# Kernel optimization log

Measured on AMD Instinct MI355X. Metric: run time of the kernel, lower is better.

## Reference

```python
import jax, jax.numpy as jnp
import numpy as np

B, T, H = 64, 1024, 1024


def setup_inputs() -> dict:
    key = jax.random.key(0)
    ks = jax.random.split(key, 8)
    s = 1.0 / np.sqrt(H)
    return {
        "spatial_feats": jax.random.normal(ks[0], (B, T, H), dtype=jnp.float32),
        "hidden_state": jax.random.normal(ks[1], (B, H), dtype=jnp.float32),
        "W_enc": jax.random.uniform(ks[2], (H, H), jnp.float32, -s, s),
        "b_enc": jax.random.uniform(ks[3], (H,), jnp.float32, -s, s),
        "W_dec": jax.random.uniform(ks[4], (H, H), jnp.float32, -s, s),
        "b_dec": jax.random.uniform(ks[5], (H,), jnp.float32, -s, s),
        "w_score": jax.random.uniform(ks[6], (H,), jnp.float32, -s, s),
        "b_score": jax.random.uniform(ks[7], (), jnp.float32, -s, s),
    }


def reference(spatial_feats, hidden_state, W_enc, b_enc, W_dec, b_dec, w_score, b_score):
    # decoder_proj(hidden_state): [B, H] -> [B, 1, H]
    dec = (jnp.einsum("bh,oh->bo", hidden_state, W_dec) + b_dec)[:, None, :]
    # encoder_proj(spatial_feats): [B, T, H]
    enc = jnp.einsum("bth,oh->bto", spatial_feats, W_enc) + b_enc
    energy = jnp.tanh(enc + dec)                      # [B, T, H]
    scores = jnp.einsum("bth,h->bt", energy, w_score) + b_score  # [B, T]
    weights = jax.nn.softmax(scores, axis=1)          # [B, T]
    context = jnp.einsum("bth,bt->bh", spatial_feats, weights)   # [B, H]
    return (context, weights)
```

## Files before the change

### kernel.cpp

```cpp
#include <hip/hip_runtime.h>
#include <hip/hip_bf16.h>
#include <math.h>


typedef __attribute__((ext_vector_type(8))) short bf16x8;
typedef __attribute__((ext_vector_type(8))) unsigned short ushort8;
typedef __attribute__((ext_vector_type(4))) float f32x4;

__device__ __forceinline__ unsigned short f2bf(float f) {
  union { float f; unsigned int u; } v; v.f = f;
  unsigned int r = v.u + 0x7FFFu + ((v.u >> 16) & 1u);
  return (unsigned short)(r >> 16);
}

__device__ __forceinline__ float bf2f(unsigned short b) {
  union { unsigned int u; float f; } v; v.u = ((unsigned int)b) << 16;
  return v.f;
}

__device__ __forceinline__ float fast_tanh(float x) {
  float e = __expf(2.0f * x);
  return 1.0f - 2.0f / (e + 1.0f);
}

__device__ __forceinline__ void gld16(const void* g, void* l) {
  __builtin_amdgcn_global_load_lds(
      (const __attribute__((address_space(1))) void*)g,
      (__attribute__((address_space(3))) void*)l, 16, 0, 0);
}

__global__ __launch_bounds__(256) void prep_kernel(
    const float* __restrict__ spatial, const float* __restrict__ hidden,
    const float* __restrict__ W_enc, const float* __restrict__ b_enc,
    const float* __restrict__ W_dec, const float* __restrict__ b_dec,
    unsigned short* __restrict__ Wbf, unsigned short* __restrict__ Abf,
    float* __restrict__ dec, int nW, int nA) {
  __shared__ float hs[1024];
  const int bid = blockIdx.x, tid = threadIdx.x;
  if (bid < nW + nA) {
    const float* src = (bid < nW) ? W_enc : spatial;
    unsigned short* dst = (bid < nW) ? Wbf : Abf;
    size_t g4 = (size_t)(bid < nW ? bid : bid - nW) * 256 + tid;
    float4 v = ((const float4*)src)[g4];
    ushort4 o;
    o.x = f2bf(v.x); o.y = f2bf(v.y); o.z = f2bf(v.z); o.w = f2bf(v.w);
    *(ushort4*)(dst + g4 * 4) = o;
    return;
  }
  const int dbid = bid - nW - nA;
  const int b = dbid >> 3, o0 = (dbid & 7) * 128;
  const int wave = tid >> 6, lane = tid & 63;
  ((float4*)hs)[tid] = ((const float4*)(hidden + (size_t)b * 1024))[tid];
  __syncthreads();
  for (int it = 0; it < 32; it++) {
    int o = o0 + it * 4 + wave;
    const float4* w4 = (const float4*)(W_dec + (size_t)o * 1024);
    float4 acc; acc.x = acc.y = acc.z = acc.w = 0.f;
    #pragma unroll
    for (int j = 0; j < 4; j++) {
      int i = j * 64 + lane;
      float4 x = ((const float4*)hs)[i], y = w4[i];
      acc.x = fmaf(x.x, y.x, acc.x);
      acc.y = fmaf(x.y, y.y, acc.y);
      acc.z = fmaf(x.z, y.z, acc.z);
      acc.w = fmaf(x.w, y.w, acc.w);
    }
    float v = (acc.x + acc.y) + (acc.z + acc.w);
    #pragma unroll
    for (int off = 1; off < 64; off <<= 1) v += __shfl_xor(v, off);
    if (lane == 0) dec[b * 1024 + o] = v + b_dec[o] + b_enc[o];
  }
}

__global__ __launch_bounds__(256) void enc_score_bf16_kernel(
    const unsigned short* __restrict__ A,
    const unsigned short* __restrict__ W,
    const float* __restrict__ dec,
    const float* __restrict__ w_score,
    float* __restrict__ scores_p)
{
  __shared__ unsigned short As[128 * 32];
  __shared__ unsigned short Bs[128 * 32];

  const int bid = blockIdx.x;
  const int m_tile = (bid >> 4) * 8 + (bid & 7);
  const int nh = (bid >> 3) & 1;
  const int m0 = m_tile * 128;
  const int tid = threadIdx.x;
  const int lane = tid & 63, wave = tid >> 6;
  const int wm = (wave >> 1) * 64, wn = (wave & 1) * 64;
  const int quad = lane >> 4, colL = lane & 15;

  const int srow = wave * 32 + (lane >> 2);
  const int scol = (lane & 3) * 8;
  const unsigned short* ga = A + (size_t)(m0 + srow) * 1024 + scol;
  unsigned short* la = As + wave * 1024;
  unsigned short* lb = Bs + wave * 1024;

  const int b = m0 >> 10;
  float rs[4][4];
  #pragma unroll
  for (int mi = 0; mi < 4; mi++)
    #pragma unroll
    for (int r = 0; r < 4; r++) rs[mi][r] = 0.f;

  for (int nt = 0; nt < 4; nt++) {
    const int n0 = (nh * 4 + nt) * 128;
    const unsigned short* gb = W + (size_t)(n0 + srow) * 1024 + scol;

    f32x4 acc[4][4];
    #pragma unroll
    for (int mi = 0; mi < 4; mi++)
      #pragma unroll
      for (int ni = 0; ni < 4; ni++)
        acc[mi][ni] = (f32x4){0.f, 0.f, 0.f, 0.f};

    for (int k0 = 0; k0 < 1024; k0 += 32) {
      gld16(ga + k0,             la);
      gld16(ga + k0 + 16 * 1024, la + 512);
      gld16(gb + k0,             lb);
      gld16(gb + k0 + 16 * 1024, lb + 512);
      __syncthreads();
      bf16x8 af[4], bfr[4];
      #pragma unroll
      for (int i = 0; i < 4; i++) {
        af[i]  = *(const bf16x8*)(As + (wm + i * 16 + colL) * 32 + quad * 8);
        bfr[i] = *(const bf16x8*)(Bs + (wn + i * 16 + colL) * 32 + quad * 8);
      }
      #pragma unroll
      for (int mi = 0; mi < 4; mi++)
        #pragma unroll
        for (int ni = 0; ni < 4; ni++)
          acc[mi][ni] = __builtin_amdgcn_mfma_f32_16x16x32_bf16(
              af[mi], bfr[ni], acc[mi][ni], 0, 0, 0);
      __syncthreads();
    }

    float decv[4], wsv[4];
    #pragma unroll
    for (int ni = 0; ni < 4; ni++) {
      int n = n0 + wn + ni * 16 + colL;
      decv[ni] = dec[b * 1024 + n];
      wsv[ni] = w_score[n];
    }
    #pragma unroll
    for (int mi = 0; mi < 4; mi++)
      #pragma unroll
      for (int ni = 0; ni < 4; ni++)
        #pragma unroll
        for (int r = 0; r < 4; r++)
          rs[mi][r] += fast_tanh(acc[mi][ni][r] + decv[ni]) * wsv[ni];
  }

  const int slot = nh * 2 + (wave & 1);
  #pragma unroll
  for (int mi = 0; mi < 4; mi++)
    #pragma unroll
    for (int r = 0; r < 4; r++) {
      float v = rs[mi][r];
      v += __shfl_xor(v, 1);
      v += __shfl_xor(v, 2);
      v += __shfl_xor(v, 4);
      v += __shfl_xor(v, 8);
      if (colL == 0)
        scores_p[slot * 65536 + m0 + wm + mi * 16 + quad * 4 + r] = v;
    }
}

__global__ __launch_bounds__(256) void enc_score_f32_kernel(
    const float* __restrict__ A, const float* __restrict__ W,
    const float* __restrict__ dec, const float* __restrict__ w_score,
    float* __restrict__ scores_p) {
  __shared__ unsigned short As[128][32];
  __shared__ unsigned short Bs[128][32];
  const int bid = blockIdx.x;
  const int n0 = (bid & 7) * 128;
  const int m0 = (bid >> 3) * 128;
  const int tid = threadIdx.x;
  const int lane = tid & 63, wave = tid >> 6;
  const int wm = (wave >> 1) * 64, wn = (wave & 1) * 64;
  const int quad = lane >> 4, colL = lane & 15;
  const int srow = tid >> 3;
  const int scol = (tid & 7) * 4;
  f32x4 acc[4][4];
  #pragma unroll
  for (int mi = 0; mi < 4; mi++)
    #pragma unroll
    for (int ni = 0; ni < 4; ni++)
      acc[mi][ni] = (f32x4){0.f, 0.f, 0.f, 0.f};
  for (int k0 = 0; k0 < 1024; k0 += 32) {
    #pragma unroll
    for (int p = 0; p < 4; p++) {
      int r = p * 32 + srow;
      float4 va = *(const float4*)(A + (size_t)(m0 + r) * 1024 + (k0 + scol));
      float4 vb = *(const float4*)(W + (size_t)(n0 + r) * 1024 + (k0 + scol));
      ushort4 pa, pb;
      pa.x = f2bf(va.x); pa.y = f2bf(va.y); pa.z = f2bf(va.z); pa.w = f2bf(va.w);
      pb.x = f2bf(vb.x); pb.y = f2bf(vb.y); pb.z = f2bf(vb.z); pb.w = f2bf(vb.w);
      *(ushort4*)(&As[r][scol]) = pa;
      *(ushort4*)(&Bs[r][scol]) = pb;
    }
    __syncthreads();
    bf16x8 af[4], bfr[4];
    #pragma unroll
    for (int i = 0; i < 4; i++) {
      af[i]  = *(const bf16x8*)(&As[wm + i * 16 + colL][quad * 8]);
      bfr[i] = *(const bf16x8*)(&Bs[wn + i * 16 + colL][quad * 8]);
    }
    #pragma unroll
    for (int mi = 0; mi < 4; mi++)
      #pragma unroll
      for (int ni = 0; ni < 4; ni++)
        acc[mi][ni] = __builtin_amdgcn_mfma_f32_16x16x32_bf16(
            af[mi], bfr[ni], acc[mi][ni], 0, 0, 0);
    __syncthreads();
  }
  const int b = m0 >> 10;
  float decv[4], wsv[4];
  #pragma unroll
  for (int ni = 0; ni < 4; ni++) {
    int n = n0 + wn + ni * 16 + colL;
    decv[ni] = dec[b * 1024 + n];
    wsv[ni] = w_score[n];
  }
  #pragma unroll
  for (int mi = 0; mi < 4; mi++) {
    float rsv[4] = {0.f, 0.f, 0.f, 0.f};
    #pragma unroll
    for (int ni = 0; ni < 4; ni++)
      #pragma unroll
      for (int r = 0; r < 4; r++)
        rsv[r] += fast_tanh(acc[mi][ni][r] + decv[ni]) * wsv[ni];
    #pragma unroll
    for (int r = 0; r < 4; r++) {
      float v = rsv[r];
      v += __shfl_xor(v, 1);
      v += __shfl_xor(v, 2);
      v += __shfl_xor(v, 4);
      v += __shfl_xor(v, 8);
      if (colL == 0)
        atomicAdd(&scores_p[m0 + wm + mi * 16 + quad * 4 + r], v);
    }
  }
}

__global__ void softmax_kernel(const float* __restrict__ scores_p,
                               float* __restrict__ weights,
                               float* __restrict__ context) {
  __shared__ float red[256];
  int b = blockIdx.x, tid = threadIdx.x;
  float4 z; z.x = z.y = z.z = z.w = 0.f;
  ((float4*)context)[blockIdx.x * 256 + tid] = z;
  float v[4];
  float mx = -1e30f;
  #pragma unroll
  for (int i = 0; i < 4; i++) {
    int m = b * 1024 + tid + i * 256;
    v[i] = scores_p[m] + scores_p[65536 + m] + scores_p[2 * 65536 + m] +
           scores_p[3 * 65536 + m];
    mx = fmaxf(mx, v[i]);
  }
  red[tid] = mx; __syncthreads();
  for (int off = 128; off > 0; off >>= 1) {
    if (tid < off) red[tid] = fmaxf(red[tid], red[tid + off]);
    __syncthreads();
  }
  mx = red[0]; __syncthreads();
  float sum = 0.f;
  #pragma unroll
  for (int i = 0; i < 4; i++) { v[i] = __expf(v[i] - mx); sum += v[i]; }
  red[tid] = sum; __syncthreads();
  for (int off = 128; off > 0; off >>= 1) {
    if (tid < off) red[tid] += red[tid + off];
    __syncthreads();
  }
  float inv = 1.0f / red[0];
  #pragma unroll
  for (int i = 0; i < 4; i++) weights[b * 1024 + tid + i * 256] = v[i] * inv;
}

__global__ void context_bf16_kernel(const unsigned short* __restrict__ Abf,
                                    const float* __restrict__ weights,
                                    float* __restrict__ context) {
  int b = blockIdx.x >> 3, tq = blockIdx.x & 7;
  int tid = threadIdx.x;
  __shared__ float wl[128];
  __shared__ float cs[128 * 8];
  if (tid < 128) wl[tid] = weights[b * 1024 + tq * 128 + tid];
  __syncthreads();
  const int hl = tid & 127, p = tid >> 7;
  const int h0 = hl * 8;
  const unsigned short* sp =
      Abf + ((size_t)(b * 1024 + tq * 128 + p)) * 1024 + h0;
  float acc[8];
  #pragma unroll
  for (int j = 0; j < 8; j++) acc[j] = 0.f;
  for (int t = 0; t < 128; t += 2) {
    float w = wl[t + p];
    ushort8 x = *(const ushort8*)(sp + (size_t)t * 1024);
    #pragma unroll
    for (int j = 0; j < 8; j++) acc[j] = fmaf(w, bf2f(x[j]), acc[j]);
  }
  if (p == 0) {
    #pragma unroll
    for (int j = 0; j < 8; j++) cs[hl * 8 + j] = acc[j];
  }
  __syncthreads();
  if (p == 1) {
    #pragma unroll
    for (int j = 0; j < 8; j++) cs[hl * 8 + j] += acc[j];
  }
  __syncthreads();
  if (p == 0) {
    #pragma unroll
    for (int j = 0; j < 8; j++)
      atomicAdd(&context[b * 1024 + h0 + j], cs[hl * 8 + j]);
  }
}

__global__ void context_f32_kernel(const float* __restrict__ spatial,
                                   const float* __restrict__ weights,
                                   float* __restrict__ context) {
  int b = blockIdx.x >> 3, tq = blockIdx.x & 7;
  int tid = threadIdx.x;
  __shared__ float wl[128];
  if (tid < 128) wl[tid] = weights[b * 1024 + tq * 128 + tid];
  __syncthreads();
  const float4* sp =
      (const float4*)(spatial + ((size_t)(b * 1024 + tq * 128)) * 1024);
  float4 acc; acc.x = acc.y = acc.z = acc.w = 0.f;
  #pragma unroll 4
  for (int t = 0; t < 128; t++) {
    float w = wl[t];
    float4 x = sp[(size_t)t * 256 + tid];
    acc.x = fmaf(w, x.x, acc.x);
    acc.y = fmaf(w, x.y, acc.y);
    acc.z = fmaf(w, x.z, acc.z);
    acc.w = fmaf(w, x.w, acc.w);
  }
  float* c = context + b * 1024 + tid * 4;
  atomicAdd(c + 0, acc.x);
  atomicAdd(c + 1, acc.y);
  atomicAdd(c + 2, acc.z);
  atomicAdd(c + 3, acc.w);
}

extern "C" void kernel_launch(void* const* d_in, const int* in_sizes, int n_in,
                              void* d_out, int out_size, void* d_ws, size_t ws_size,
                              hipStream_t stream) {
  const float* spatial  = (const float*)d_in[0];
  const float* hidden   = (const float*)d_in[1];
  const float* W_enc    = (const float*)d_in[2];
  const float* b_enc    = (const float*)d_in[3];
  const float* W_dec    = (const float*)d_in[4];
  const float* b_dec    = (const float*)d_in[5];
  const float* w_score  = (const float*)d_in[6];

  float* out      = (float*)d_out;
  float* context  = out;
  float* weights  = out + 65536;

  float* scores_p = (float*)d_ws;
  float* dec      = scores_p + 4 * 65536;
  unsigned short* Wbf = (unsigned short*)(dec + 65536);
  unsigned short* Abf = Wbf + 1024 * 1024;

  const size_t need =
      4ull * 65536 * 4 + 65536 * 4 + 2ull * 1024 * 1024 + 2ull * 65536 * 1024;

  if (ws_size >= need) {
    const int nW = 1024, nA = 65536;
    prep_kernel<<<nW + nA + 512, 256, 0, stream>>>(
        spatial, hidden, W_enc, b_enc, W_dec, b_dec, Wbf, Abf, dec, nW, nA);
    enc_score_bf16_kernel<<<1024, 256, 0, stream>>>(Abf, Wbf, dec, w_score,
                                                    scores_p);
    softmax_kernel<<<64, 256, 0, stream>>>(scores_p, weights, context);
    context_bf16_kernel<<<512, 256, 0, stream>>>(Abf, weights, context);
  } else {
    hipMemsetAsync(scores_p, 0, 4 * 65536 * sizeof(float), stream);
    prep_kernel<<<512, 256, 0, stream>>>(
        spatial, hidden, W_enc, b_enc, W_dec, b_dec, nullptr, nullptr, dec,
        0, 0);
    enc_score_f32_kernel<<<4096, 256, 0, stream>>>(spatial, W_enc, dec,
                                                   w_score, scores_p);
    softmax_kernel<<<64, 256, 0, stream>>>(scores_p, weights, context);
    context_f32_kernel<<<512, 256, 0, stream>>>(spatial, weights, context);
  }
}
```

Measured before the change: 672.4 us.

## Split bf16 enc-score GEMM into one 128x128 tile per block with 16 partial-score slots

The bf16 encoder-score kernel no longer loops over four N tiles per block. Each block now computes a single 128x128 output tile, so the grid grows from 1024 to 4096 blocks, and every wave writes its own partial row score into one of 16 slots. The softmax then sums all 16 slots, and the f32 fallback drops its atomics and memset in favour of the same slot scheme. The aim is more parallelism and a shorter per-block critical path. The cost is more A-tile reloads from memory (each A row tile is now read by 8 blocks instead of 2), a larger partial-score workspace and more reads in the softmax.

```diff
diff --git a/kernel.cpp b/kernel.cpp
--- a/kernel.cpp
+++ b/kernel.cpp
@@ -83,9 +83,8 @@
   __shared__ unsigned short Bs[128 * 32];
 
   const int bid = blockIdx.x;
-  const int m_tile = (bid >> 4) * 8 + (bid & 7);
-  const int nh = (bid >> 3) & 1;
-  const int m0 = m_tile * 128;
+  const int n0 = (bid & 7) * 128;
+  const int m0 = (bid >> 3) * 128;
   const int tid = threadIdx.x;
   const int lane = tid & 63, wave = tid >> 6;
   const int wm = (wave >> 1) * 64, wn = (wave & 1) * 64;
@@ -94,70 +93,58 @@
   const int srow = wave * 32 + (lane >> 2);
   const int scol = (lane & 3) * 8;
   const unsigned short* ga = A + (size_t)(m0 + srow) * 1024 + scol;
+  const unsigned short* gb = W + (size_t)(n0 + srow) * 1024 + scol;
   unsigned short* la = As + wave * 1024;
   unsigned short* lb = Bs + wave * 1024;
 
-  const int b = m0 >> 10;
-  float rs[4][4];
+  f32x4 acc[4][4];
   #pragma unroll
   for (int mi = 0; mi < 4; mi++)
     #pragma unroll
-    for (int r = 0; r < 4; r++) rs[mi][r] = 0.f;
-
-  for (int nt = 0; nt < 4; nt++) {
-    const int n0 = (nh * 4 + nt) * 128;
-    const unsigned short* gb = W + (size_t)(n0 + srow) * 1024 + scol;
-
-    f32x4 acc[4][4];
+    for (int ni = 0; ni < 4; ni++)
+      acc[mi][ni] = (f32x4){0.f, 0.f, 0.f, 0.f};
+
+  for (int k0 = 0; k0 < 1024; k0 += 32) {
+    gld16(ga + k0,             la);
+    gld16(ga + k0 + 16 * 1024, la + 512);
+    gld16(gb + k0,             lb);
+    gld16(gb + k0 + 16 * 1024, lb + 512);
+    __syncthreads();
+    bf16x8 af[4], bfr[4];
+    #pragma unroll
+    for (int i = 0; i < 4; i++) {
+      af[i]  = *(const bf16x8*)(As + (wm + i * 16 + colL) * 32 + quad * 8);
+      bfr[i] = *(const bf16x8*)(Bs + (wn + i * 16 + colL) * 32 + quad * 8);
+    }
     #pragma unroll
     for (int mi = 0; mi < 4; mi++)
       #pragma unroll
       for (int ni = 0; ni < 4; ni++)
-        acc[mi][ni] = (f32x4){0.f, 0.f, 0.f, 0.f};
-
-    for (int k0 = 0; k0 < 1024; k0 += 32) {
-      gld16(ga + k0,             la);
-      gld16(ga + k0 + 16 * 1024, la + 512);
-      gld16(gb + k0,             lb);
-      gld16(gb + k0 + 16 * 1024, lb + 512);
-      __syncthreads();
-      bf16x8 af[4], bfr[4];
+        acc[mi][ni] = __builtin_amdgcn_mfma_f32_16x16x32_bf16(
+            af[mi], bfr[ni], acc[mi][ni], 0, 0, 0);
+    __syncthreads();
+  }
+
+  const int b = m0 >> 10;
+  float decv[4], wsv[4];
+  #pragma unroll
+  for (int ni = 0; ni < 4; ni++) {
+    int n = n0 + wn + ni * 16 + colL;
+    decv[ni] = dec[b * 1024 + n];
+    wsv[ni] = w_score[n];
+  }
+  const int slot = (bid & 7) * 2 + (wave & 1);
+  #pragma unroll
+  for (int mi = 0; mi < 4; mi++) {
+    float rs[4] = {0.f, 0.f, 0.f, 0.f};
+    #pragma unroll
+    for (int ni = 0; ni < 4; ni++)
       #pragma unroll
-      for (int i = 0; i < 4; i++) {
-        af[i]  = *(const bf16x8*)(As + (wm + i * 16 + colL) * 32 + quad * 8);
-        bfr[i] = *(const bf16x8*)(Bs + (wn + i * 16 + colL) * 32 + quad * 8);
-      }
-      #pragma unroll
-      for (int mi = 0; mi < 4; mi++)
-        #pragma unroll
-        for (int ni = 0; ni < 4; ni++)
-          acc[mi][ni] = __builtin_amdgcn_mfma_f32_16x16x32_bf16(
-              af[mi], bfr[ni], acc[mi][ni], 0, 0, 0);
-      __syncthreads();
-    }
-
-    float decv[4], wsv[4];
-    #pragma unroll
-    for (int ni = 0; ni < 4; ni++) {
-      int n = n0 + wn + ni * 16 + colL;
-      decv[ni] = dec[b * 1024 + n];
-      wsv[ni] = w_score[n];
-    }
-    #pragma unroll
-    for (int mi = 0; mi < 4; mi++)
-      #pragma unroll
-      for (int ni = 0; ni < 4; ni++)
-        #pragma unroll
-        for (int r = 0; r < 4; r++)
-          rs[mi][r] += fast_tanh(acc[mi][ni][r] + decv[ni]) * wsv[ni];
-  }
-
-  const int slot = nh * 2 + (wave & 1);
-  #pragma unroll
-  for (int mi = 0; mi < 4; mi++)
+      for (int r = 0; r < 4; r++)
+        rs[r] += fast_tanh(acc[mi][ni][r] + decv[ni]) * wsv[ni];
     #pragma unroll
     for (int r = 0; r < 4; r++) {
-      float v = rs[mi][r];
+      float v = rs[r];
       v += __shfl_xor(v, 1);
       v += __shfl_xor(v, 2);
       v += __shfl_xor(v, 4);
@@ -165,6 +152,7 @@
       if (colL == 0)
         scores_p[slot * 65536 + m0 + wm + mi * 16 + quad * 4 + r] = v;
     }
+  }
 }
 
 __global__ __launch_bounds__(256) void enc_score_f32_kernel(
@@ -223,6 +211,7 @@
     decv[ni] = dec[b * 1024 + n];
     wsv[ni] = w_score[n];
   }
+  const int slot = (bid & 7) * 2 + (wave & 1);
   #pragma unroll
   for (int mi = 0; mi < 4; mi++) {
     float rsv[4] = {0.f, 0.f, 0.f, 0.f};
@@ -239,7 +228,7 @@
       v += __shfl_xor(v, 4);
       v += __shfl_xor(v, 8);
       if (colL == 0)
-        atomicAdd(&scores_p[m0 + wm + mi * 16 + quad * 4 + r], v);
+        scores_p[slot * 65536 + m0 + wm + mi * 16 + quad * 4 + r] = v;
     }
   }
 }
@@ -256,8 +245,10 @@
   #pragma unroll
   for (int i = 0; i < 4; i++) {
     int m = b * 1024 + tid + i * 256;
-    v[i] = scores_p[m] + scores_p[65536 + m] + scores_p[2 * 65536 + m] +
-           scores_p[3 * 65536 + m];
+    float s = 0.f;
+    #pragma unroll
+    for (int sl = 0; sl < 16; sl++) s += scores_p[sl * 65536 + m];
+    v[i] = s;
     mx = fmaxf(mx, v[i]);
   }
   red[tid] = mx; __syncthreads();
@@ -361,23 +352,22 @@
   float* weights  = out + 65536;
 
   float* scores_p = (float*)d_ws;
-  float* dec      = scores_p + 4 * 65536;
+  float* dec      = scores_p + 16 * 65536;
   unsigned short* Wbf = (unsigned short*)(dec + 65536);
   unsigned short* Abf = Wbf + 1024 * 1024;
 
   const size_t need =
-      4ull * 65536 * 4 + 65536 * 4 + 2ull * 1024 * 1024 + 2ull * 65536 * 1024;
+      16ull * 65536 * 4 + 65536 * 4 + 2ull * 1024 * 1024 + 2ull * 65536 * 1024;
 
   if (ws_size >= need) {
     const int nW = 1024, nA = 65536;
     prep_kernel<<<nW + nA + 512, 256, 0, stream>>>(
         spatial, hidden, W_enc, b_enc, W_dec, b_dec, Wbf, Abf, dec, nW, nA);
-    enc_score_bf16_kernel<<<1024, 256, 0, stream>>>(Abf, Wbf, dec, w_score,
+    enc_score_bf16_kernel<<<4096, 256, 0, stream>>>(Abf, Wbf, dec, w_score,
                                                     scores_p);
     softmax_kernel<<<64, 256, 0, stream>>>(scores_p, weights, context);
     context_bf16_kernel<<<512, 256, 0, stream>>>(Abf, weights, context);
   } else {
-    hipMemsetAsync(scores_p, 0, 4 * 65536 * sizeof(float), stream);
     prep_kernel<<<512, 256, 0, stream>>>(
         spatial, hidden, W_enc, b_enc, W_dec, b_dec, nullptr, nullptr, dec,
         0, 0);
```

Measured after the change: 636.1 us. -5.4%, faster.
